# Optimization experiments

Measured on AMD Instinct MI355X. Metric: run time of the kernel, lower is better.

The kernel has to match this reference:

```python
import jax, jax.numpy as jnp
import numpy as np
from jax.scipy.special import digamma

N, D, K = 32768, 64, 64


def setup_inputs() -> dict:
    key = jax.random.key(0)
    k1, k2, k3, k4, k5, k6, k7 = jax.random.split(key, 7)
    X = jax.random.normal(k1, (N, D), dtype=jnp.float32)
    means = jax.random.normal(k2, (K, D), dtype=jnp.float32)
    # Upper-triangular precision Cholesky factors with strictly positive diagonal
    # (matches solve_triangular(L, I).T from the torch code).
    off = jnp.triu(jax.random.normal(k3, (K, D, D), dtype=jnp.float32) * 0.05, 1)
    diag = jnp.exp(jax.random.normal(k4, (K, D), dtype=jnp.float32) * 0.1)
    precisions_chol = off + jax.vmap(jnp.diag)(diag)
    weight_concentration = jax.random.uniform(k5, (2, K), dtype=jnp.float32, minval=0.5, maxval=5.0)
    # degrees_of_freedom must be > D - 1 so digamma args stay positive
    degrees_of_freedom = jnp.float32(D) + jax.random.uniform(k6, (K,), dtype=jnp.float32, minval=1.0, maxval=50.0)
    mean_precision = jax.random.uniform(k7, (K,), dtype=jnp.float32, minval=0.5, maxval=10.0)
    return {"X": X, "means": means, "precisions_chol": precisions_chol,
            "weight_concentration": weight_concentration,
            "degrees_of_freedom": degrees_of_freedom, "mean_precision": mean_precision}


def _weighted_log_prob(X, means, precisions_chol, weight_concentration,
                       degrees_of_freedom, mean_precision):
    n_features = X.shape[1]
    # log|prec_chol_k| = sum of log of diagonal entries
    log_det = jnp.sum(jnp.log(jnp.diagonal(precisions_chol, axis1=1, axis2=2)), axis=1)  # [K]
    # whitened residuals: y[n,k,:] = X[n] @ P_k - mu_k @ P_k
    XP = jnp.einsum('nd,kde->nke', X, precisions_chol)            # [N,K,D]
    muP = jnp.einsum('kd,kde->ke', means, precisions_chol)        # [K,D]
    sq = jnp.sum(jnp.square(XP - muP[None]), axis=-1)             # [N,K]
    log2pi = jnp.log(jnp.float32(2.0 * np.pi))
    log_gauss = -0.5 * (n_features * log2pi + sq) + log_det[None]
    # Bayesian corrections
    log_gauss = log_gauss - 0.5 * n_features * jnp.log(degrees_of_freedom)[None]
    i = jnp.arange(n_features, dtype=jnp.float32)
    log_lambda = n_features * jnp.log(jnp.float32(2.0)) + jnp.sum(
        digamma(0.5 * (degrees_of_freedom[None, :] - i[:, None])), axis=0)  # [K]
    log_prob = log_gauss + 0.5 * (log_lambda - n_features / mean_precision)[None]
    # stick-breaking log weights (dirichlet_process)
    a, b = weight_concentration[0], weight_concentration[1]
    dsum = digamma(a + b)
    log_w = digamma(a) - dsum + jnp.concatenate(
        [jnp.zeros((1,), dtype=X.dtype), jnp.cumsum(digamma(b) - dsum)[:-1]])
    return log_prob + log_w[None]


def reference(X, means, precisions_chol, weight_concentration,
              degrees_of_freedom, mean_precision):
    wlp = _weighted_log_prob(X, means, precisions_chol, weight_concentration,
                             degrees_of_freedom, mean_precision)
    return jnp.argmax(wlp, axis=1)
```

## Files before the change

kernel.cpp:

```cpp
#include <hip/hip_runtime.h>
#include <math.h>

#define N_ROWS 32768
#define DIM 64
#define KCOMP 64
#define KSPLIT 8
#define KLOCAL 8
#define THREADS 256
#define PREP_THREADS 256
#define RT 4
#define ROWS_PER_WAVE 64
#define ROWS_PER_BLOCK 256
#define ROWGROUPS (N_ROWS / ROWS_PER_BLOCK)

#define PT_K_BYTES 12288

#define LOG2PI_D 1.8378770664093454836

typedef _Float16 f16x8 __attribute__((ext_vector_type(8)));
typedef float f32x4 __attribute__((ext_vector_type(4)));

#define AS1 __attribute__((address_space(1)))
#define AS3 __attribute__((address_space(3)))

__device__ __forceinline__ void async_copy16(const char* g, char* l) {
  __builtin_amdgcn_global_load_lds((const AS1 unsigned int*)g,
                                   (AS3 unsigned int*)l, 16, 0, 0);
}

__device__ __forceinline__ double digamma_d(double x) {
  double r = 0.0;
  while (x < 6.0) { r -= 1.0 / x; x += 1.0; }
  double inv = 1.0 / x;
  double inv2 = inv * inv;
  double s = log(x) - 0.5 * inv
      - inv2 * (1.0/12.0 - inv2 * (1.0/120.0 - inv2 * (1.0/252.0
      - inv2 * (1.0/240.0 - inv2 * (1.0/132.0)))));
  return r + s;
}

__global__ void prep1_kernel(const float* __restrict__ means,
                             const float* __restrict__ P,
                             const float* __restrict__ wc,
                             const float* __restrict__ dof,
                             const float* __restrict__ mp,
                             char*   __restrict__ Pt,
                             float*  __restrict__ muP,
                             double* __restrict__ t_arr,
                             double* __restrict__ g_arr,
                             double* __restrict__ pc_arr,
                             uint4*  __restrict__ packed4,
                             uint4*  __restrict__ cnt4)
{
  __shared__ float lds[DIM][DIM + 1];
  const int k = blockIdx.x;
  const int t = threadIdx.x;
  const float* Pk = P + k * DIM * DIM;

  const uint4 z4 = {0u, 0u, 0u, 0u};
  packed4[k * PREP_THREADS + t] = z4;
  if (k == 0 && t < 64) cnt4[t] = z4;

  for (int i = t; i < DIM * DIM; i += PREP_THREADS)
    lds[i >> 6][i & 63] = Pk[i];
  __syncthreads();

  char* dst = Pt + (size_t)k * PT_K_BYTES;
#pragma unroll
  for (int cc = 0; cc < 3; ++cc) {
    int cid  = cc * PREP_THREADS + t;
    int slot = cid >> 7;
    int sel  = (cid >> 6) & 1;
    int lane = cid & 63;
    int et = slot < 2 ? slot : 2 + ((slot - 2) >> 1);
    int c  = slot < 2 ? 0    : ((slot - 2) & 1);
    int m = lane & 15, q = lane >> 4;
    int e = et * 16 + m;
    int d0 = c * 32 + q * 8;
    f16x8 o;
#pragma unroll
    for (int j = 0; j < 8; ++j) {
      float v = lds[d0 + j][e];
      _Float16 h = (_Float16)v;
      o[j] = sel ? (_Float16)(v - (float)h) : h;
    }
    *(f16x8*)(dst + cid * 16) = o;
  }

  if (t < 64) {
    const int i = t;
    const float* mk = means + k * DIM;
    float acc = 0.f;
#pragma unroll 8
    for (int d = 0; d < DIM; ++d) acc = fmaf(mk[d], lds[d][i], acc);
    muP[k * DIM + i] = acc;

    double dofk = (double)dof[k];
    double s1 = digamma_d(0.5 * (dofk - (double)i));
    double s2 = log((double)lds[i][i]);
#pragma unroll
    for (int off = 32; off > 0; off >>= 1) {
      s1 += __shfl_down(s1, off);
      s2 += __shfl_down(s2, off);
    }
    if (i == 0) {
      double ak = (double)wc[k], bk = (double)wc[KCOMP + k];
      double dgab = digamma_d(ak + bk);
      double log_lambda = (double)DIM * log(2.0) + s1;
      double pc = s2
                - 0.5 * (double)DIM * LOG2PI_D
                - 0.5 * (double)DIM * log(dofk)
                + 0.5 * (log_lambda - (double)DIM / (double)mp[k]);
      t_arr[k] = digamma_d(bk) - dgab;
      g_arr[k] = digamma_d(ak) - dgab;
      pc_arr[k] = pc;
    }
  }
}

__global__ __launch_bounds__(THREADS, 4) void main_kernel(
    const float* __restrict__ X,
    const char*  __restrict__ Pt,
    const float* __restrict__ muP,
    const double* __restrict__ t_arr,
    const double* __restrict__ g_arr,
    const double* __restrict__ pc_arr,
    unsigned long long* __restrict__ packed,
    int* __restrict__ cnt,
    int* __restrict__ out)
{
  __shared__ uint4 bbuf[2][PT_K_BYTES / 16];
  __shared__ __align__(16) float mup_lds[KLOCAL * DIM];
  __shared__ float cvec_lds[KCOMP];
  __shared__ int is_last;

  const int tid  = threadIdx.x;
  const int wave = tid >> 6;
  const int lane = tid & 63;
  const int m    = lane & 15;
  const int q    = lane >> 4;
  const int ks   = blockIdx.y;
  const int rowbase = blockIdx.x * ROWS_PER_BLOCK + wave * ROWS_PER_WAVE;
  const int k0   = ks * KLOCAL;

  {
    const char* src = Pt + (size_t)k0 * PT_K_BYTES;
#pragma unroll
    for (int i = 0; i < 3; ++i) {
      const int g = wave * 3 + i;
      async_copy16(src + (g << 10) + (lane << 4),
                   (char*)&bbuf[0][g << 6]);
    }
  }

  if (tid < 64) {
    double t = t_arr[tid];
    double s = t;
#pragma unroll
    for (int off = 1; off < 64; off <<= 1) {
      double v = __shfl_up(s, off);
      if (tid >= off) s += v;
    }
    cvec_lds[tid] = (float)(pc_arr[tid] + g_arr[tid] + (s - t));
  }
  for (int i = tid; i < KLOCAL * DIM; i += THREADS)
    mup_lds[i] = muP[ks * KLOCAL * DIM + i];

  f16x8 ahi[RT][2], alo[RT][2];
#pragma unroll
  for (int rt = 0; rt < RT; ++rt) {
    int row = rowbase + rt * 16 + m;
    const float* xp = X + row * DIM;
#pragma unroll
    for (int c = 0; c < 2; ++c) {
      const float4* xq4 = (const float4*)(xp + c * 32 + q * 8);
      float4 v0 = xq4[0], v1 = xq4[1];
      float xv[8] = {v0.x, v0.y, v0.z, v0.w, v1.x, v1.y, v1.z, v1.w};
      f16x8 h, l;
#pragma unroll
      for (int j = 0; j < 8; ++j) {
        _Float16 hv = (_Float16)xv[j];
        h[j] = hv;
        l[j] = (_Float16)(xv[j] - (float)hv);
      }
      ahi[rt][c] = h;
      alo[rt][c] = l;
    }
  }

  __syncthreads();

  float best = -INFINITY;
  int   bidx = 0;

  for (int ki = 0; ki < KLOCAL; ++ki) {
    const int k = k0 + ki;
    const int p = ki & 1;

    if (ki + 1 < KLOCAL) {
      const char* src = Pt + (size_t)(k + 1) * PT_K_BYTES;
#pragma unroll
      for (int i = 0; i < 3; ++i) {
        const int g = wave * 3 + i;
        async_copy16(src + (g << 10) + (lane << 4),
                     (char*)&bbuf[1 - p][g << 6]);
      }
    }

    const char* lb = (const char*)bbuf[p];
    const float ck = cvec_lds[k];
    float sq[RT];
#pragma unroll
    for (int rt = 0; rt < RT; ++rt) sq[rt] = 0.f;

    __builtin_amdgcn_s_setprio(1);
#pragma unroll
    for (int et = 0; et < 4; ++et) {
      const f32x4 mv4 = *(const f32x4*)&mup_lds[(ki << 6) + (et << 4) + (q << 2)];
      const f32x4 mi = -mv4;
      f32x4 acc[RT];
#pragma unroll
      for (int rt = 0; rt < RT; ++rt) acc[rt] = mi;

      const int nc = (et < 2) ? 1 : 2;
#pragma unroll
      for (int c = 0; c < nc; ++c) {
        const int slot = (et < 2) ? et : (2 + (et - 2) * 2 + c);
        const char* bp = lb + (slot << 11) + (lane << 4);
        f16x8 bh = *(const f16x8*)bp;
        f16x8 bl = *(const f16x8*)(bp + 1024);
#pragma unroll
        for (int rt = 0; rt < RT; ++rt) {
          acc[rt] = __builtin_amdgcn_mfma_f32_16x16x32_f16(bh, ahi[rt][c], acc[rt], 0, 0, 0);
          acc[rt] = __builtin_amdgcn_mfma_f32_16x16x32_f16(bl, ahi[rt][c], acc[rt], 0, 0, 0);
          acc[rt] = __builtin_amdgcn_mfma_f32_16x16x32_f16(bh, alo[rt][c], acc[rt], 0, 0, 0);
        }
      }
#pragma unroll
      for (int rt = 0; rt < RT; ++rt)
#pragma unroll
        for (int r = 0; r < 4; ++r)
          sq[rt] = fmaf(acc[rt][r], acc[rt][r], sq[rt]);
    }
    __builtin_amdgcn_s_setprio(0);

    float f0, f1, f2, f3;
    {
      float v0 = sq[0] + __shfl_xor(sq[0], 16); f0 = v0 + __shfl_xor(v0, 32);
      float v1 = sq[1] + __shfl_xor(sq[1], 16); f1 = v1 + __shfl_xor(v1, 32);
      float v2 = sq[2] + __shfl_xor(sq[2], 16); f2 = v2 + __shfl_xor(v2, 32);
      float v3 = sq[3] + __shfl_xor(sq[3], 16); f3 = v3 + __shfl_xor(v3, 32);
    }
    float z01 = (q & 1) ? f1 : f0;
    float z23 = (q & 1) ? f3 : f2;
    float z   = (q & 2) ? z23 : z01;

    float wv = fmaf(-0.5f, z, ck);
    if (wv > best || (wv == best && k < bidx)) { best = wv; bidx = k; }

    __syncthreads();
  }

  {
    int row = rowbase + lane;
    unsigned int b = __float_as_uint(best);
    unsigned int u = (b & 0x80000000u) ? ~b : (b | 0x80000000u);
    unsigned long long pkd = ((unsigned long long)u << 32)
                           | (unsigned long long)(63 - bidx);
    atomicMax(&packed[row], pkd);
  }
  __builtin_amdgcn_s_waitcnt(0);
  __syncthreads();
  if (tid == 0) {
    int old = atomicAdd(&cnt[blockIdx.x], 1);
    is_last = (old == KSPLIT - 1);
  }
  __syncthreads();
  if (is_last) {
    int n = blockIdx.x * ROWS_PER_BLOCK + tid;
    unsigned long long pv = __hip_atomic_load(&packed[n], __ATOMIC_RELAXED,
                                              __HIP_MEMORY_SCOPE_AGENT);
    out[n] = 63 - (int)(pv & 63ull);
  }
}

extern "C" void kernel_launch(void* const* d_in, const int* in_sizes, int n_in,
                              void* d_out, int out_size, void* d_ws, size_t ws_size,
                              hipStream_t stream) {
  const float* X     = (const float*)d_in[0];
  const float* means = (const float*)d_in[1];
  const float* P     = (const float*)d_in[2];
  const float* wc    = (const float*)d_in[3];
  const float* dof   = (const float*)d_in[4];
  const float* mp    = (const float*)d_in[5];
  int* out = (int*)d_out;

  char* wsb = (char*)d_ws;
  float*  muP    = (float*)(wsb);
  double* t_arr  = (double*)(wsb + 16640);
  double* g_arr  = (double*)(wsb + 17152);
  double* pc_arr = (double*)(wsb + 17664);
  int*    cnt    = (int*)(wsb + 20480);
  unsigned long long* packed = (unsigned long long*)(wsb + 24576);
  char*   Pt     = wsb + 294912;

  prep1_kernel<<<KCOMP, PREP_THREADS, 0, stream>>>(means, P, wc, dof, mp, Pt,
                                                   muP, t_arr, g_arr, pc_arr,
                                                   (uint4*)packed, (uint4*)cnt);

  dim3 grid(ROWGROUPS, KSPLIT);
  main_kernel<<<grid, THREADS, 0, stream>>>(X, Pt, muP, t_arr, g_arr, pc_arr,
                                            packed, cnt, out);
}
```

Measured before the change: 105.3 us.

## Switch Mahalanobis GEMM from 16x16x32 to 32x32x16 MFMA tiles

Replaces the 16x16x32 f16 MFMA tiling with 32x32x16 MFMA tiles: each wave handles two 32-row tiles against 32-column output-dimension tiles. The host-side packing of the precision matrix and the per-lane X fragment loads are rearranged to match the new operand layout, and the cross-lane reduction of squared residuals drops to one shuffle per tile. The aim is to cut the number of MFMA issues, B-operand LDS reads and shuffles per component. The cost is larger accumulators (two 16-wide vectors), which raises register pressure.

```diff
diff --git a/kernel.cpp b/kernel.cpp
--- a/kernel.cpp
+++ b/kernel.cpp
@@ -8,7 +8,6 @@
 #define KLOCAL 8
 #define THREADS 256
 #define PREP_THREADS 256
-#define RT 4
 #define ROWS_PER_WAVE 64
 #define ROWS_PER_BLOCK 256
 #define ROWGROUPS (N_ROWS / ROWS_PER_BLOCK)
@@ -19,6 +18,7 @@
 
 typedef _Float16 f16x8 __attribute__((ext_vector_type(8)));
 typedef float f32x4 __attribute__((ext_vector_type(4)));
+typedef float f32x16 __attribute__((ext_vector_type(16)));
 
 #define AS1 __attribute__((address_space(1)))
 #define AS3 __attribute__((address_space(3)))
@@ -72,17 +72,17 @@
     int slot = cid >> 7;
     int sel  = (cid >> 6) & 1;
     int lane = cid & 63;
-    int et = slot < 2 ? slot : 2 + ((slot - 2) >> 1);
-    int c  = slot < 2 ? 0    : ((slot - 2) & 1);
-    int m = lane & 15, q = lane >> 4;
-    int e = et * 16 + m;
-    int d0 = c * 32 + q * 8;
+    int ET = slot < 2 ? 0 : 1;
+    int ds = slot < 2 ? slot : slot - 2;
+    int m32 = lane & 31, h = lane >> 5;
+    int e  = ET * 32 + m32;
+    int d0 = ds * 16 + h * 8;
     f16x8 o;
 #pragma unroll
     for (int j = 0; j < 8; ++j) {
       float v = lds[d0 + j][e];
-      _Float16 h = (_Float16)v;
-      o[j] = sel ? (_Float16)(v - (float)h) : h;
+      _Float16 hh = (_Float16)v;
+      o[j] = sel ? (_Float16)(v - (float)hh) : hh;
     }
     *(f16x8*)(dst + cid * 16) = o;
   }
@@ -137,8 +137,8 @@
   const int tid  = threadIdx.x;
   const int wave = tid >> 6;
   const int lane = tid & 63;
-  const int m    = lane & 15;
-  const int q    = lane >> 4;
+  const int m32  = lane & 31;
+  const int h    = lane >> 5;
   const int ks   = blockIdx.y;
   const int rowbase = blockIdx.x * ROWS_PER_BLOCK + wave * ROWS_PER_WAVE;
   const int k0   = ks * KLOCAL;
@@ -166,25 +166,25 @@
   for (int i = tid; i < KLOCAL * DIM; i += THREADS)
     mup_lds[i] = muP[ks * KLOCAL * DIM + i];
 
-  f16x8 ahi[RT][2], alo[RT][2];
-#pragma unroll
-  for (int rt = 0; rt < RT; ++rt) {
-    int row = rowbase + rt * 16 + m;
+  f16x8 xhi[2][4], xlo[2][4];
+#pragma unroll
+  for (int nt = 0; nt < 2; ++nt) {
+    int row = rowbase + nt * 32 + m32;
     const float* xp = X + row * DIM;
 #pragma unroll
-    for (int c = 0; c < 2; ++c) {
-      const float4* xq4 = (const float4*)(xp + c * 32 + q * 8);
+    for (int ds = 0; ds < 4; ++ds) {
+      const float4* xq4 = (const float4*)(xp + ds * 16 + h * 8);
       float4 v0 = xq4[0], v1 = xq4[1];
       float xv[8] = {v0.x, v0.y, v0.z, v0.w, v1.x, v1.y, v1.z, v1.w};
-      f16x8 h, l;
+      f16x8 hh, ll;
 #pragma unroll
       for (int j = 0; j < 8; ++j) {
         _Float16 hv = (_Float16)xv[j];
-        h[j] = hv;
-        l[j] = (_Float16)(xv[j] - (float)hv);
-      }
-      ahi[rt][c] = h;
-      alo[rt][c] = l;
+        hh[j] = hv;
+        ll[j] = (_Float16)(xv[j] - (float)hv);
+      }
+      xhi[nt][ds] = hh;
+      xlo[nt][ds] = ll;
     }
   }
 
@@ -209,51 +209,47 @@
 
     const char* lb = (const char*)bbuf[p];
     const float ck = cvec_lds[k];
-    float sq[RT];
-#pragma unroll
-    for (int rt = 0; rt < RT; ++rt) sq[rt] = 0.f;
+    float sq0 = 0.f, sq1 = 0.f;
 
     __builtin_amdgcn_s_setprio(1);
 #pragma unroll
-    for (int et = 0; et < 4; ++et) {
-      const f32x4 mv4 = *(const f32x4*)&mup_lds[(ki << 6) + (et << 4) + (q << 2)];
-      const f32x4 mi = -mv4;
-      f32x4 acc[RT];
-#pragma unroll
-      for (int rt = 0; rt < RT; ++rt) acc[rt] = mi;
-
-      const int nc = (et < 2) ? 1 : 2;
-#pragma unroll
-      for (int c = 0; c < nc; ++c) {
-        const int slot = (et < 2) ? et : (2 + (et - 2) * 2 + c);
+    for (int ET = 0; ET < 2; ++ET) {
+      f32x16 a0, a1;
+#pragma unroll
+      for (int g = 0; g < 4; ++g) {
+        const f32x4 mv = *(const f32x4*)&mup_lds[(ki << 6) + (ET << 5)
+                                                 + (g << 3) + (h << 2)];
+#pragma unroll
+        for (int i = 0; i < 4; ++i) a0[g * 4 + i] = -mv[i];
+      }
+      a1 = a0;
+
+#pragma unroll
+      for (int ds = 0; ds < 4; ++ds) {
+        if (ET == 0 && ds >= 2) continue;
+        const int slot = (ET == 0) ? ds : 2 + ds;
         const char* bp = lb + (slot << 11) + (lane << 4);
-        f16x8 bh = *(const f16x8*)bp;
-        f16x8 bl = *(const f16x8*)(bp + 1024);
-#pragma unroll
-        for (int rt = 0; rt < RT; ++rt) {
-          acc[rt] = __builtin_amdgcn_mfma_f32_16x16x32_f16(bh, ahi[rt][c], acc[rt], 0, 0, 0);
-          acc[rt] = __builtin_amdgcn_mfma_f32_16x16x32_f16(bl, ahi[rt][c], acc[rt], 0, 0, 0);
-          acc[rt] = __builtin_amdgcn_mfma_f32_16x16x32_f16(bh, alo[rt][c], acc[rt], 0, 0, 0);
-        }
-      }
-#pragma unroll
-      for (int rt = 0; rt < RT; ++rt)
-#pragma unroll
-        for (int r = 0; r < 4; ++r)
-          sq[rt] = fmaf(acc[rt][r], acc[rt][r], sq[rt]);
+        f16x8 ph = *(const f16x8*)bp;
+        f16x8 pl = *(const f16x8*)(bp + 1024);
+        a0 = __builtin_amdgcn_mfma_f32_32x32x16_f16(ph, xhi[0][ds], a0, 0, 0, 0);
+        a0 = __builtin_amdgcn_mfma_f32_32x32x16_f16(pl, xhi[0][ds], a0, 0, 0, 0);
+        a0 = __builtin_amdgcn_mfma_f32_32x32x16_f16(ph, xlo[0][ds], a0, 0, 0, 0);
+        a1 = __builtin_amdgcn_mfma_f32_32x32x16_f16(ph, xhi[1][ds], a1, 0, 0, 0);
+        a1 = __builtin_amdgcn_mfma_f32_32x32x16_f16(pl, xhi[1][ds], a1, 0, 0, 0);
+        a1 = __builtin_amdgcn_mfma_f32_32x32x16_f16(ph, xlo[1][ds], a1, 0, 0, 0);
+      }
+
+#pragma unroll
+      for (int r = 0; r < 16; ++r) {
+        sq0 = fmaf(a0[r], a0[r], sq0);
+        sq1 = fmaf(a1[r], a1[r], sq1);
+      }
     }
     __builtin_amdgcn_s_setprio(0);
 
-    float f0, f1, f2, f3;
-    {
-      float v0 = sq[0] + __shfl_xor(sq[0], 16); f0 = v0 + __shfl_xor(v0, 32);
-      float v1 = sq[1] + __shfl_xor(sq[1], 16); f1 = v1 + __shfl_xor(v1, 32);
-      float v2 = sq[2] + __shfl_xor(sq[2], 16); f2 = v2 + __shfl_xor(v2, 32);
-      float v3 = sq[3] + __shfl_xor(sq[3], 16); f3 = v3 + __shfl_xor(v3, 32);
-    }
-    float z01 = (q & 1) ? f1 : f0;
-    float z23 = (q & 1) ? f3 : f2;
-    float z   = (q & 2) ? z23 : z01;
+    float z0 = sq0 + __shfl_xor(sq0, 32);
+    float z1 = sq1 + __shfl_xor(sq1, 32);
+    float z  = (lane < 32) ? z0 : z1;
 
     float wv = fmaf(-0.5f, z, ck);
     if (wv > best || (wv == best && k < bidx)) { best = wv; bidx = k; }
```

Result: slower. 108.1 us (+2.6%).
